# Optimization experiments

Hardware: AMD Instinct MI355X
Metric: run time of the kernel (lower is better)

Reference implementation:

```python
import jax, jax.numpy as jnp
import numpy as np

N = 50000
E = 800000
FEAT = 512
HID = 256
CLS = 40
EPS = 1e-5


def setup_inputs() -> dict:
    key = jax.random.key(0)
    ks = jax.random.split(key, 8)
    x = jax.random.normal(ks[0], (N, FEAT), dtype=jnp.float32)
    edge_index = jax.random.randint(ks[1], (2, E), 0, N, dtype=jnp.int64)
    s = 0.05
    return {
        "x": x,
        "edge_index": edge_index,
        "W1": jax.random.normal(ks[2], (FEAT, HID), dtype=jnp.float32) * s,
        "b1": jnp.zeros((HID,), jnp.float32),
        "W2": jax.random.normal(ks[3], (HID, HID), dtype=jnp.float32) * s,
        "b2": jnp.zeros((HID,), jnp.float32),
        "W3": jax.random.normal(ks[4], (HID, CLS), dtype=jnp.float32) * s,
        "b3": jnp.zeros((CLS,), jnp.float32),
        "gamma": jnp.ones((HID,), jnp.float32),
        "beta": jnp.zeros((HID,), jnp.float32),
        "run_mean": jnp.zeros((HID,), jnp.float32),
        "run_var": jnp.ones((HID,), jnp.float32),
    }


def _edge_norm(edge_index):
    # add self-loops, then symmetric normalization D^-1/2 (A+I) D^-1/2
    loop = jnp.arange(N, dtype=edge_index.dtype)
    src = jnp.concatenate([edge_index[0], loop])
    dst = jnp.concatenate([edge_index[1], loop])
    deg = jax.ops.segment_sum(jnp.ones_like(dst, jnp.float32), dst, num_segments=N)
    inv_sqrt = jnp.where(deg > 0, jax.lax.rsqrt(jnp.maximum(deg, 1.0)), 0.0)
    norm = inv_sqrt[src] * inv_sqrt[dst]  # [E+N]
    return src, dst, norm


def _gcn_conv(x, W, b, src, dst, norm):
    h = x @ W                               # [N, out]
    msg = h[src] * norm[:, None]            # gather + scale, [E+N, out]
    out = jax.ops.segment_sum(msg, dst, num_segments=N)
    return out + b


def _bn_relu(x, gamma, beta, mean, var):
    return jax.nn.relu((x - mean) * jax.lax.rsqrt(var + EPS) * gamma + beta)


def reference(x, edge_index, W1, b1, W2, b2, W3, b3, gamma, beta, run_mean, run_var):
    src, dst, norm = _edge_norm(edge_index)
    h = _gcn_conv(x, W1, b1, src, dst, norm)
    h = _bn_relu(h, gamma, beta, run_mean, run_var)
    h = _gcn_conv(h, W2, b2, src, dst, norm)
    h = _bn_relu(h, gamma, beta, run_mean, run_var)
    h = _gcn_conv(h, W3, b3, src, dst, norm)
    return h
```

## Files before the change

kernel.cpp:

```cpp
#include <hip/hip_runtime.h>
#include <cstdint>
#include <cstddef>

#define FEAT 512
#define HID 256
#define CLS 40
#define EPS 1e-5f

typedef __attribute__((ext_vector_type(8))) short short8;
typedef __attribute__((ext_vector_type(4))) float f32x4v;


__device__ __forceinline__ unsigned short f2bf(float f) {
    union { float f; unsigned u; } v; v.f = f;
    unsigned r = v.u + 0x7FFF + ((v.u >> 16) & 1);
    return (unsigned short)(r >> 16);
}
__device__ __forceinline__ float bf2f(unsigned short h) {
    union { unsigned u; float f; } v; v.u = ((unsigned)h) << 16;
    return v.f;
}

typedef const __attribute__((address_space(1))) unsigned int* gas_ptr;
typedef __attribute__((address_space(3))) unsigned int* las_ptr;
__device__ __forceinline__ void lds_load16(const void* g, void* l) {
    __builtin_amdgcn_global_load_lds((gas_ptr)g, (las_ptr)l, 16, 0, 0);
}

__device__ __forceinline__ void split_f8(float4 a, float4 b, short8& hi, short8& lo) {
    float f[8] = {a.x, a.y, a.z, a.w, b.x, b.y, b.z, b.w};
#pragma unroll
    for (int i = 0; i < 8; ++i) {
        unsigned short h = f2bf(f[i]);
        hi[i] = (short)h;
        lo[i] = (short)f2bf(f[i] - bf2f(h));
    }
}

__device__ __forceinline__ float4 f4add(float4 a, float4 b) {
    return make_float4(a.x + b.x, a.y + b.y, a.z + b.z, a.w + b.w);
}

__device__ __forceinline__ void accum_bf4(float4& a, ushort4 v) {
    a.x += bf2f(v.x); a.y += bf2f(v.y); a.z += bf2f(v.z); a.w += bf2f(v.w);
}


__global__ void zero_kernel(int* counts, int* fillpos, int n) {
    int i = blockIdx.x * 256 + threadIdx.x;
    if (i < n) { counts[i] = 0; fillpos[i] = 0; }
}

__global__ void hist_kernel(const int* __restrict__ dst, int* __restrict__ counts, int E) {
    int e = blockIdx.x * 256 + threadIdx.x;
    if (e < E) atomicAdd(&counts[dst[e]], 1);
}

__global__ void scan_block_kernel(const int* __restrict__ counts, int* __restrict__ row_ptr,
                                  int* __restrict__ blocksums, int n) {
    __shared__ int s[256];
    int tid = threadIdx.x;
    int i = blockIdx.x * 256 + tid;
    int v = (i < n) ? counts[i] : 0;
    s[tid] = v; __syncthreads();
    for (int off = 1; off < 256; off <<= 1) {
        int t = (tid >= off) ? s[tid - off] : 0;
        __syncthreads();
        s[tid] += t;
        __syncthreads();
    }
    if (i < n) row_ptr[i] = s[tid] - v;
    if (tid == 255) blocksums[blockIdx.x] = s[255];
}

__global__ void scan_sums_kernel(const int* __restrict__ blocksums, int* __restrict__ blockoffs, int nb) {
    __shared__ int s[256];
    int tid = threadIdx.x;
    int v = (tid < nb) ? blocksums[tid] : 0;
    s[tid] = v; __syncthreads();
    for (int off = 1; off < 256; off <<= 1) {
        int t = (tid >= off) ? s[tid - off] : 0;
        __syncthreads();
        s[tid] += t;
        __syncthreads();
    }
    blockoffs[tid] = s[tid] - v;
}

__global__ void finalize_rowptr_kernel(int* __restrict__ row_ptr, const int* __restrict__ blockoffs,
                                       const int* __restrict__ counts, float* __restrict__ inv_sqrt,
                                       int n, int E) {
    int i = blockIdx.x * 256 + threadIdx.x;
    if (i < n) {
        row_ptr[i] += blockoffs[i >> 8];
        inv_sqrt[i] = rsqrtf((float)(counts[i] + 1));
    }
    if (i == 0) row_ptr[n] = E;
}

__global__ void fill_kernel(const int* __restrict__ src, const int* __restrict__ dst,
                            const int* __restrict__ row_ptr, int* __restrict__ fillpos,
                            int* __restrict__ src_sorted, int E) {
    int e = blockIdx.x * 256 + threadIdx.x;
    if (e < E) {
        int d = dst[e];
        int pos = row_ptr[d] + atomicAdd(&fillpos[d], 1);
        src_sorted[pos] = src[e];
    }
}


__global__ void cvt_w_kernel(const float* __restrict__ W, unsigned short* __restrict__ hi,
                             unsigned short* __restrict__ lo, int K, int Ncol) {
    int idx = blockIdx.x * 256 + threadIdx.x;
    if (idx >= K * Ncol) return;
    int k = idx / Ncol, n = idx % Ncol;
    float f = W[idx];
    unsigned short h = f2bf(f);
    hi[(size_t)n * K + k] = h;
    lo[(size_t)n * K + k] = f2bf(f - bf2f(h));
}


template<bool A_SPLIT>
__global__ __launch_bounds__(256) void gemm_mfma_kernel(
        const float* __restrict__ Afp,
        const unsigned short* __restrict__ gAhi, const unsigned short* __restrict__ gAlo,
        const unsigned short* __restrict__ Wthi, const unsigned short* __restrict__ Wtlo,
        const float* __restrict__ inv_sqrt, unsigned short* __restrict__ C,
        int M, int K, int Ncol) {
    __shared__ unsigned short AhiL[4096], AloL[4096], BhiL[4096], BloL[4096];
    const int tid  = threadIdx.x;
    const int lane = tid & 63;
    const int w    = tid >> 6;
    const int wr   = w >> 1, wc = w & 1;
    const int lm   = lane & 15;
    const int lk8  = (lane >> 4) * 8;
    const int bm   = blockIdx.x * 128;
    const int bn   = blockIdx.y * 128;

    f32x4v acc[4][4] = {};

    int nc0 = bn + 16 * (2 * w) + lm;
    int nc1 = bn + 16 * (2 * w + 1) + lm;
    const unsigned short* gB_h0 = Wthi + (size_t)nc0 * K + lk8;
    const unsigned short* gB_h1 = Wthi + (size_t)nc1 * K + lk8;
    const unsigned short* gB_l0 = Wtlo + (size_t)nc0 * K + lk8;
    const unsigned short* gB_l1 = Wtlo + (size_t)nc1 * K + lk8;

    int ar0 = bm + 16 * (2 * w) + lm;     if (ar0 >= M) ar0 = M - 1;
    int ar1 = bm + 16 * (2 * w + 1) + lm; if (ar1 >= M) ar1 = M - 1;
    const unsigned short* gA_h0 = gAhi ? gAhi + (size_t)ar0 * K + lk8 : nullptr;
    const unsigned short* gA_h1 = gAhi ? gAhi + (size_t)ar1 * K + lk8 : nullptr;
    const unsigned short* gA_l0 = gAlo ? gAlo + (size_t)ar0 * K + lk8 : nullptr;
    const unsigned short* gA_l1 = gAlo ? gAlo + (size_t)ar1 * K + lk8 : nullptr;

    const int cb = tid >> 5;
    const int cs = tid & 31;
    int crow = bm + 16 * cb + (cs & 15); if (crow >= M) crow = M - 1;
    const int ck = (cs >> 4) * 8;
    const float* Abase = Afp ? Afp + (size_t)crow * K + ck : nullptr;
    unsigned short* ldsA_hi = &AhiL[cb * 512 + 8 * cs];
    unsigned short* ldsA_lo = &AloL[cb * 512 + 8 * cs];

    for (int k0 = 0; k0 < K; k0 += 32) {
        if (A_SPLIT) {
            lds_load16(gA_h0 + k0, &AhiL[(2 * w) * 512]);
            lds_load16(gA_h1 + k0, &AhiL[(2 * w + 1) * 512]);
            lds_load16(gA_l0 + k0, &AloL[(2 * w) * 512]);
            lds_load16(gA_l1 + k0, &AloL[(2 * w + 1) * 512]);
        } else {
            float4 a0 = *(const float4*)(Abase + k0);
            float4 a1 = *(const float4*)(Abase + k0 + 4);
            float4 c0 = *(const float4*)(Abase + k0 + 16);
            float4 c1 = *(const float4*)(Abase + k0 + 20);
            short8 h0, l0, h1, l1;
            split_f8(a0, a1, h0, l0);
            split_f8(c0, c1, h1, l1);
            *(short8*)ldsA_hi         = h0;
            *(short8*)(ldsA_hi + 256) = h1;
            *(short8*)ldsA_lo         = l0;
            *(short8*)(ldsA_lo + 256) = l1;
        }
        lds_load16(gB_h0 + k0, &BhiL[(2 * w) * 512]);
        lds_load16(gB_h1 + k0, &BhiL[(2 * w + 1) * 512]);
        lds_load16(gB_l0 + k0, &BloL[(2 * w) * 512]);
        lds_load16(gB_l1 + k0, &BloL[(2 * w + 1) * 512]);
        __syncthreads();

        short8 ah[4], av[4], bh[4], bv[4];
#pragma unroll
        for (int i = 0; i < 4; ++i) {
            int ao = (wr * 4 + i) * 512 + lane * 8;
            int bo = (wc * 4 + i) * 512 + lane * 8;
            ah[i] = *(const short8*)&AhiL[ao];
            av[i] = *(const short8*)&AloL[ao];
            bh[i] = *(const short8*)&BhiL[bo];
            bv[i] = *(const short8*)&BloL[bo];
        }
#pragma unroll
        for (int i = 0; i < 4; ++i)
#pragma unroll
            for (int j = 0; j < 4; ++j) {
                acc[i][j] = __builtin_amdgcn_mfma_f32_16x16x32_bf16(ah[i], bh[j], acc[i][j], 0, 0, 0);
                acc[i][j] = __builtin_amdgcn_mfma_f32_16x16x32_bf16(av[i], bh[j], acc[i][j], 0, 0, 0);
                acc[i][j] = __builtin_amdgcn_mfma_f32_16x16x32_bf16(ah[i], bv[j], acc[i][j], 0, 0, 0);
            }
        __syncthreads();
    }

    const int orow_base = bm + wr * 64;
    const int ocol_base = bn + wc * 64 + lm;
    const int rq = (lane >> 4) * 4;
#pragma unroll
    for (int i = 0; i < 4; ++i) {
#pragma unroll
        for (int r = 0; r < 4; ++r) {
            int row = orow_base + i * 16 + rq + r;
            if (row >= M) continue;
            float s = inv_sqrt[row];
            size_t rb = (size_t)row * Ncol;
#pragma unroll
            for (int j = 0; j < 4; ++j)
                C[rb + ocol_base + j * 16] = f2bf(acc[i][j][r] * s);
        }
    }
}


__global__ __launch_bounds__(256) void gemm_scaled_hl_kernel(
        const unsigned short* __restrict__ Ahi, const unsigned short* __restrict__ Alo,
        const float* __restrict__ W,
        const float* __restrict__ inv_sqrt, float* __restrict__ C,
        int M, int K, int Ncol) {
    __shared__ float As[16][64];
    __shared__ float Ws[16][64];
    int tid = threadIdx.x;
    int tm = tid >> 4;
    int tn = tid & 15;
    int bm = blockIdx.x * 64;
    int bn = blockIdx.y * 64;

    float acc[4][4] = {};

    int lr = tid >> 2;
    int lc = (tid & 3) << 2;
    int wr = tid >> 4;
    int wc = (tid & 15) << 2;
    int arow = bm + lr;
    bool aok = arow < M;
    bool wok = (bn + wc) < Ncol;
    const unsigned short* AhiRow = Ahi + (size_t)arow * K + lc;
    const unsigned short* AloRow = Alo + (size_t)arow * K + lc;

    for (int k0 = 0; k0 < K; k0 += 16) {
        float4 av = make_float4(0.f, 0.f, 0.f, 0.f);
        if (aok) {
            ushort4 hv = *(const ushort4*)(AhiRow + k0);
            ushort4 lv = *(const ushort4*)(AloRow + k0);
            av.x = bf2f(hv.x) + bf2f(lv.x);
            av.y = bf2f(hv.y) + bf2f(lv.y);
            av.z = bf2f(hv.z) + bf2f(lv.z);
            av.w = bf2f(hv.w) + bf2f(lv.w);
        }
        As[lc + 0][lr] = av.x; As[lc + 1][lr] = av.y;
        As[lc + 2][lr] = av.z; As[lc + 3][lr] = av.w;

        float4 wv = make_float4(0.f, 0.f, 0.f, 0.f);
        if (wok) wv = *(const float4*)(W + (size_t)(k0 + wr) * Ncol + bn + wc);
        *(float4*)&Ws[wr][wc] = wv;
        __syncthreads();

#pragma unroll
        for (int k = 0; k < 16; ++k) {
            const float4 a4 = *(const float4*)&As[k][tm << 2];
            const float4 b4 = *(const float4*)&Ws[k][tn << 2];
            float a[4] = {a4.x, a4.y, a4.z, a4.w};
            float b[4] = {b4.x, b4.y, b4.z, b4.w};
#pragma unroll
            for (int i = 0; i < 4; ++i)
#pragma unroll
                for (int j = 0; j < 4; ++j)
                    acc[i][j] = fmaf(a[i], b[j], acc[i][j]);
        }
        __syncthreads();
    }

#pragma unroll
    for (int i = 0; i < 4; ++i) {
        int row = bm + (tm << 2) + i;
        if (row >= M) continue;
        float s = inv_sqrt[row];
        int col = bn + (tn << 2);
        if (col < Ncol) {
            float4 o = make_float4(acc[i][0] * s, acc[i][1] * s, acc[i][2] * s, acc[i][3] * s);
            *(float4*)&C[(size_t)row * Ncol + col] = o;
        }
    }
}


__global__ __launch_bounds__(256) void agg_bn_hl_kernel(
        const unsigned short* __restrict__ g, const int* __restrict__ row_ptr,
        const int* __restrict__ srcs, const float* __restrict__ inv_sqrt,
        const float* __restrict__ bias, const float* __restrict__ gamma,
        const float* __restrict__ beta, const float* __restrict__ mean,
        const float* __restrict__ var,
        unsigned short* __restrict__ out_hi, unsigned short* __restrict__ out_lo, int n) {
    int node = (blockIdx.x << 2) + (threadIdx.x >> 6);
    int lane = threadIdx.x & 63;
    if (node >= n) return;
    const ushort4* gp = (const ushort4*)g;
    float4 acc0 = make_float4(0.f, 0.f, 0.f, 0.f);
    float4 acc1 = make_float4(0.f, 0.f, 0.f, 0.f);
    accum_bf4(acc0, gp[(size_t)node * 64 + lane]);
    int beg = row_ptr[node];
    int cnt = row_ptr[node + 1] - beg;

    for (int base = 0; base < cnt; base += 64) {
        int m = cnt - base; if (m > 64) m = 64;
        int idx = (lane < m) ? srcs[beg + base + lane] : 0;
        int j = 0;
        for (; j + 8 <= m; j += 8) {
            int s0 = __shfl(idx, j + 0), s1 = __shfl(idx, j + 1);
            int s2 = __shfl(idx, j + 2), s3 = __shfl(idx, j + 3);
            int s4 = __shfl(idx, j + 4), s5 = __shfl(idx, j + 5);
            int s6 = __shfl(idx, j + 6), s7 = __shfl(idx, j + 7);
            ushort4 v0 = gp[(size_t)s0 * 64 + lane];
            ushort4 v1 = gp[(size_t)s1 * 64 + lane];
            ushort4 v2 = gp[(size_t)s2 * 64 + lane];
            ushort4 v3 = gp[(size_t)s3 * 64 + lane];
            ushort4 v4 = gp[(size_t)s4 * 64 + lane];
            ushort4 v5 = gp[(size_t)s5 * 64 + lane];
            ushort4 v6 = gp[(size_t)s6 * 64 + lane];
            ushort4 v7 = gp[(size_t)s7 * 64 + lane];
            accum_bf4(acc0, v0); accum_bf4(acc0, v1);
            accum_bf4(acc0, v2); accum_bf4(acc0, v3);
            accum_bf4(acc1, v4); accum_bf4(acc1, v5);
            accum_bf4(acc1, v6); accum_bf4(acc1, v7);
        }
        for (; j < m; ++j) {
            int s = __shfl(idx, j);
            accum_bf4(acc0, gp[(size_t)s * 64 + lane]);
        }
    }
    float4 acc = f4add(acc0, acc1);

    float inv = inv_sqrt[node];
    float4 b4  = ((const float4*)bias)[lane];
    float4 ga4 = ((const float4*)gamma)[lane];
    float4 be4 = ((const float4*)beta)[lane];
    float4 m4  = ((const float4*)mean)[lane];
    float4 v4  = ((const float4*)var)[lane];
    float4 o;
    o.x = fmaxf((acc.x * inv + b4.x - m4.x) * (ga4.x * rsqrtf(v4.x + EPS)) + be4.x, 0.f);
    o.y = fmaxf((acc.y * inv + b4.y - m4.y) * (ga4.y * rsqrtf(v4.y + EPS)) + be4.y, 0.f);
    o.z = fmaxf((acc.z * inv + b4.z - m4.z) * (ga4.z * rsqrtf(v4.z + EPS)) + be4.z, 0.f);
    o.w = fmaxf((acc.w * inv + b4.w - m4.w) * (ga4.w * rsqrtf(v4.w + EPS)) + be4.w, 0.f);
    ushort4 oh, ol;
    oh.x = f2bf(o.x); ol.x = f2bf(o.x - bf2f(oh.x));
    oh.y = f2bf(o.y); ol.y = f2bf(o.y - bf2f(oh.y));
    oh.z = f2bf(o.z); ol.z = f2bf(o.z - bf2f(oh.z));
    oh.w = f2bf(o.w); ol.w = f2bf(o.w - bf2f(oh.w));
    ((ushort4*)out_hi)[(size_t)node * 64 + lane] = oh;
    ((ushort4*)out_lo)[(size_t)node * 64 + lane] = ol;
}


__global__ __launch_bounds__(256) void agg_final_kernel(
        const float* __restrict__ g, const int* __restrict__ row_ptr,
        const int* __restrict__ srcs, const float* __restrict__ inv_sqrt,
        const float* __restrict__ bias, float* __restrict__ out, int n) {
    int node = (blockIdx.x << 2) + (threadIdx.x >> 6);
    int lane = threadIdx.x & 63;
    if (node >= n) return;
    int flane = (lane < CLS) ? lane : 0;
    float acc0 = g[(size_t)node * CLS + flane];
    float acc1 = 0.f;
    int beg = row_ptr[node];
    int cnt = row_ptr[node + 1] - beg;

    for (int base = 0; base < cnt; base += 64) {
        int m = cnt - base; if (m > 64) m = 64;
        int idx = (lane < m) ? srcs[beg + base + lane] : 0;
        int j = 0;
        for (; j + 8 <= m; j += 8) {
            int s0 = __shfl(idx, j + 0), s1 = __shfl(idx, j + 1);
            int s2 = __shfl(idx, j + 2), s3 = __shfl(idx, j + 3);
            int s4 = __shfl(idx, j + 4), s5 = __shfl(idx, j + 5);
            int s6 = __shfl(idx, j + 6), s7 = __shfl(idx, j + 7);
            float v0 = g[(size_t)s0 * CLS + flane];
            float v1 = g[(size_t)s1 * CLS + flane];
            float v2 = g[(size_t)s2 * CLS + flane];
            float v3 = g[(size_t)s3 * CLS + flane];
            float v4 = g[(size_t)s4 * CLS + flane];
            float v5 = g[(size_t)s5 * CLS + flane];
            float v6 = g[(size_t)s6 * CLS + flane];
            float v7 = g[(size_t)s7 * CLS + flane];
            acc0 += (v0 + v1) + (v2 + v3);
            acc1 += (v4 + v5) + (v6 + v7);
        }
        for (; j < m; ++j) {
            int s = __shfl(idx, j);
            acc0 += g[(size_t)s * CLS + flane];
        }
    }
    if (lane < CLS)
        out[(size_t)node * CLS + lane] = (acc0 + acc1) * inv_sqrt[node] + bias[lane];
}


extern "C" void kernel_launch(void* const* d_in, const int* in_sizes, int n_in,
                              void* d_out, int out_size, void* d_ws, size_t ws_size,
                              hipStream_t stream) {
    const float* x     = (const float*)d_in[0];
    const int*   edges = (const int*)d_in[1];
    const float* W1    = (const float*)d_in[2];
    const float* b1    = (const float*)d_in[3];
    const float* W2    = (const float*)d_in[4];
    const float* b2    = (const float*)d_in[5];
    const float* W3    = (const float*)d_in[6];
    const float* b3    = (const float*)d_in[7];
    const float* gamma = (const float*)d_in[8];
    const float* beta  = (const float*)d_in[9];
    const float* mean  = (const float*)d_in[10];
    const float* var   = (const float*)d_in[11];

    const int N = in_sizes[0] / FEAT;
    const int E = in_sizes[1] / 2;
    const int* src = edges;
    const int* dst = edges + E;

    char* ws = (char*)d_ws;
    auto alloc = [&](size_t bytes) -> char* {
        char* p = ws;
        ws += (bytes + 255) & ~(size_t)255;
        return p;
    };
    int*   counts     = (int*)  alloc((size_t)N * 4);
    int*   fillpos    = (int*)  alloc((size_t)N * 4);
    int*   row_ptr    = (int*)  alloc((size_t)(N + 1) * 4);
    int*   blocksums  = (int*)  alloc(256 * 4);
    int*   blockoffs  = (int*)  alloc(256 * 4);
    float* inv_sqrt   = (float*)alloc((size_t)N * 4);
    int*   src_sorted = (int*)  alloc((size_t)E * 4);
    unsigned short* w1hi = (unsigned short*)alloc((size_t)FEAT * HID * 2);
    unsigned short* w1lo = (unsigned short*)alloc((size_t)FEAT * HID * 2);
    unsigned short* w2hi = (unsigned short*)alloc((size_t)HID * HID * 2);
    unsigned short* w2lo = (unsigned short*)alloc((size_t)HID * HID * 2);
    unsigned short* g    = (unsigned short*)alloc((size_t)N * HID * 2);
    unsigned short* h_hi = (unsigned short*)alloc((size_t)N * HID * 2);
    unsigned short* h_lo = (unsigned short*)alloc((size_t)N * HID * 2);

    int nb = (N + 255) / 256;
    int eb = (E + 255) / 256;

    zero_kernel<<<nb, 256, 0, stream>>>(counts, fillpos, N);
    hist_kernel<<<eb, 256, 0, stream>>>(dst, counts, E);
    scan_block_kernel<<<nb, 256, 0, stream>>>(counts, row_ptr, blocksums, N);
    scan_sums_kernel<<<1, 256, 0, stream>>>(blocksums, blockoffs, nb);
    finalize_rowptr_kernel<<<nb, 256, 0, stream>>>(row_ptr, blockoffs, counts, inv_sqrt, N, E);
    fill_kernel<<<eb, 256, 0, stream>>>(src, dst, row_ptr, fillpos, src_sorted, E);

    cvt_w_kernel<<<(FEAT * HID + 255) / 256, 256, 0, stream>>>(W1, w1hi, w1lo, FEAT, HID);
    cvt_w_kernel<<<(HID * HID + 255) / 256, 256, 0, stream>>>(W2, w2hi, w2lo, HID, HID);

    dim3 mfma_grid((N + 127) / 128, HID / 128);
    dim3 gemm3_grid((N + 63) / 64, 1);
    dim3 agg_grid((N + 3) / 4);

    gemm_mfma_kernel<false><<<mfma_grid, 256, 0, stream>>>(
        x, nullptr, nullptr, w1hi, w1lo, inv_sqrt, g, N, FEAT, HID);
    agg_bn_hl_kernel<<<agg_grid, 256, 0, stream>>>(g, row_ptr, src_sorted, inv_sqrt,
                                                   b1, gamma, beta, mean, var, h_hi, h_lo, N);
    gemm_mfma_kernel<true><<<mfma_grid, 256, 0, stream>>>(
        nullptr, h_hi, h_lo, w2hi, w2lo, inv_sqrt, g, N, HID, HID);
    agg_bn_hl_kernel<<<agg_grid, 256, 0, stream>>>(g, row_ptr, src_sorted, inv_sqrt,
                                                   b2, gamma, beta, mean, var, h_hi, h_lo, N);
    float* g3 = (float*)g;
    gemm_scaled_hl_kernel<<<gemm3_grid, 256, 0, stream>>>(h_hi, h_lo, W3, inv_sqrt, g3, N, HID, CLS);
    agg_final_kernel<<<agg_grid, 256, 0, stream>>>(g3, row_ptr, src_sorted, inv_sqrt,
                                                   b3, (float*)d_out, N);
}
```

Before: 550.0 us.

## Pre-convert x to bf16 in a separate pass and drop A low-part MFMA in layer 1

Adds a standalone kernel that converts x to bf16 (high part only) into a reused buffer. The first GEMM then loads A through global_load_lds instead of converting fp32 in the inner loop, and drops the A-low correction MFMA and its LDS buffer. This cuts the per-tile conversion ALU work, a third of the layer-1 MFMAs, and LDS footprint. In exchange it adds an extra read and write pass over x and loses the low-order bits of x, so layer-1 precision drops.

```diff
diff --git a/kernel.cpp b/kernel.cpp
--- a/kernel.cpp
+++ b/kernel.cpp
@@ -25,16 +25,6 @@
 typedef __attribute__((address_space(3))) unsigned int* las_ptr;
 __device__ __forceinline__ void lds_load16(const void* g, void* l) {
     __builtin_amdgcn_global_load_lds((gas_ptr)g, (las_ptr)l, 16, 0, 0);
-}
-
-__device__ __forceinline__ void split_f8(float4 a, float4 b, short8& hi, short8& lo) {
-    float f[8] = {a.x, a.y, a.z, a.w, b.x, b.y, b.z, b.w};
-#pragma unroll
-    for (int i = 0; i < 8; ++i) {
-        unsigned short h = f2bf(f[i]);
-        hi[i] = (short)h;
-        lo[i] = (short)f2bf(f[i] - bf2f(h));
-    }
 }
 
 __device__ __forceinline__ float4 f4add(float4 a, float4 b) {
@@ -122,14 +112,29 @@
 }
 
 
+__global__ __launch_bounds__(256) void cvt_x_kernel(const float* __restrict__ x,
+                                                    unsigned short* __restrict__ out, int total8) {
+    int i = blockIdx.x * 256 + threadIdx.x;
+    if (i >= total8) return;
+    const float4* xp = (const float4*)x;
+    float4 a = xp[2 * i], b = xp[2 * i + 1];
+    float f[8] = {a.x, a.y, a.z, a.w, b.x, b.y, b.z, b.w};
+    short8 h;
+#pragma unroll
+    for (int j = 0; j < 8; ++j) h[j] = (short)f2bf(f[j]);
+    ((short8*)out)[i] = h;
+}
+
+
 template<bool A_SPLIT>
 __global__ __launch_bounds__(256) void gemm_mfma_kernel(
-        const float* __restrict__ Afp,
         const unsigned short* __restrict__ gAhi, const unsigned short* __restrict__ gAlo,
         const unsigned short* __restrict__ Wthi, const unsigned short* __restrict__ Wtlo,
         const float* __restrict__ inv_sqrt, unsigned short* __restrict__ C,
         int M, int K, int Ncol) {
-    __shared__ unsigned short AhiL[4096], AloL[4096], BhiL[4096], BloL[4096];
+    __shared__ unsigned short AhiL[4096];
+    __shared__ unsigned short AloL[A_SPLIT ? 4096 : 4];
+    __shared__ unsigned short BhiL[4096], BloL[4096];
     const int tid  = threadIdx.x;
     const int lane = tid & 63;
     const int w    = tid >> 6;
@@ -150,37 +155,17 @@
 
     int ar0 = bm + 16 * (2 * w) + lm;     if (ar0 >= M) ar0 = M - 1;
     int ar1 = bm + 16 * (2 * w + 1) + lm; if (ar1 >= M) ar1 = M - 1;
-    const unsigned short* gA_h0 = gAhi ? gAhi + (size_t)ar0 * K + lk8 : nullptr;
-    const unsigned short* gA_h1 = gAhi ? gAhi + (size_t)ar1 * K + lk8 : nullptr;
-    const unsigned short* gA_l0 = gAlo ? gAlo + (size_t)ar0 * K + lk8 : nullptr;
-    const unsigned short* gA_l1 = gAlo ? gAlo + (size_t)ar1 * K + lk8 : nullptr;
-
-    const int cb = tid >> 5;
-    const int cs = tid & 31;
-    int crow = bm + 16 * cb + (cs & 15); if (crow >= M) crow = M - 1;
-    const int ck = (cs >> 4) * 8;
-    const float* Abase = Afp ? Afp + (size_t)crow * K + ck : nullptr;
-    unsigned short* ldsA_hi = &AhiL[cb * 512 + 8 * cs];
-    unsigned short* ldsA_lo = &AloL[cb * 512 + 8 * cs];
+    const unsigned short* gA_h0 = gAhi + (size_t)ar0 * K + lk8;
+    const unsigned short* gA_h1 = gAhi + (size_t)ar1 * K + lk8;
+    const unsigned short* gA_l0 = A_SPLIT ? gAlo + (size_t)ar0 * K + lk8 : nullptr;
+    const unsigned short* gA_l1 = A_SPLIT ? gAlo + (size_t)ar1 * K + lk8 : nullptr;
 
     for (int k0 = 0; k0 < K; k0 += 32) {
+        lds_load16(gA_h0 + k0, &AhiL[(2 * w) * 512]);
+        lds_load16(gA_h1 + k0, &AhiL[(2 * w + 1) * 512]);
         if (A_SPLIT) {
-            lds_load16(gA_h0 + k0, &AhiL[(2 * w) * 512]);
-            lds_load16(gA_h1 + k0, &AhiL[(2 * w + 1) * 512]);
             lds_load16(gA_l0 + k0, &AloL[(2 * w) * 512]);
             lds_load16(gA_l1 + k0, &AloL[(2 * w + 1) * 512]);
-        } else {
-            float4 a0 = *(const float4*)(Abase + k0);
-            float4 a1 = *(const float4*)(Abase + k0 + 4);
-            float4 c0 = *(const float4*)(Abase + k0 + 16);
-            float4 c1 = *(const float4*)(Abase + k0 + 20);
-            short8 h0, l0, h1, l1;
-            split_f8(a0, a1, h0, l0);
-            split_f8(c0, c1, h1, l1);
-            *(short8*)ldsA_hi         = h0;
-            *(short8*)(ldsA_hi + 256) = h1;
-            *(short8*)ldsA_lo         = l0;
-            *(short8*)(ldsA_lo + 256) = l1;
         }
         lds_load16(gB_h0 + k0, &BhiL[(2 * w) * 512]);
         lds_load16(gB_h1 + k0, &BhiL[(2 * w + 1) * 512]);
@@ -194,7 +179,7 @@
             int ao = (wr * 4 + i) * 512 + lane * 8;
             int bo = (wc * 4 + i) * 512 + lane * 8;
             ah[i] = *(const short8*)&AhiL[ao];
-            av[i] = *(const short8*)&AloL[ao];
+            if (A_SPLIT) av[i] = *(const short8*)&AloL[ao];
             bh[i] = *(const short8*)&BhiL[bo];
             bv[i] = *(const short8*)&BloL[bo];
         }
@@ -203,7 +188,8 @@
 #pragma unroll
             for (int j = 0; j < 4; ++j) {
                 acc[i][j] = __builtin_amdgcn_mfma_f32_16x16x32_bf16(ah[i], bh[j], acc[i][j], 0, 0, 0);
-                acc[i][j] = __builtin_amdgcn_mfma_f32_16x16x32_bf16(av[i], bh[j], acc[i][j], 0, 0, 0);
+                if (A_SPLIT)
+                    acc[i][j] = __builtin_amdgcn_mfma_f32_16x16x32_bf16(av[i], bh[j], acc[i][j], 0, 0, 0);
                 acc[i][j] = __builtin_amdgcn_mfma_f32_16x16x32_bf16(ah[i], bv[j], acc[i][j], 0, 0, 0);
             }
         __syncthreads();
@@ -451,6 +437,7 @@
     unsigned short* g    = (unsigned short*)alloc((size_t)N * HID * 2);
     unsigned short* h_hi = (unsigned short*)alloc((size_t)N * HID * 2);
     unsigned short* h_lo = (unsigned short*)alloc((size_t)N * HID * 2);
+    unsigned short* xbf  = h_hi;
 
     int nb = (N + 255) / 256;
     int eb = (E + 255) / 256;
@@ -464,17 +451,19 @@
 
     cvt_w_kernel<<<(FEAT * HID + 255) / 256, 256, 0, stream>>>(W1, w1hi, w1lo, FEAT, HID);
     cvt_w_kernel<<<(HID * HID + 255) / 256, 256, 0, stream>>>(W2, w2hi, w2lo, HID, HID);
+    int total8 = N * FEAT / 8;
+    cvt_x_kernel<<<(total8 + 255) / 256, 256, 0, stream>>>(x, xbf, total8);
 
     dim3 mfma_grid((N + 127) / 128, HID / 128);
     dim3 gemm3_grid((N + 63) / 64, 1);
     dim3 agg_grid((N + 3) / 4);
 
     gemm_mfma_kernel<false><<<mfma_grid, 256, 0, stream>>>(
-        x, nullptr, nullptr, w1hi, w1lo, inv_sqrt, g, N, FEAT, HID);
+        xbf, nullptr, w1hi, w1lo, inv_sqrt, g, N, FEAT, HID);
     agg_bn_hl_kernel<<<agg_grid, 256, 0, stream>>>(g, row_ptr, src_sorted, inv_sqrt,
                                                    b1, gamma, beta, mean, var, h_hi, h_lo, N);
     gemm_mfma_kernel<true><<<mfma_grid, 256, 0, stream>>>(
-        nullptr, h_hi, h_lo, w2hi, w2lo, inv_sqrt, g, N, HID, HID);
+        h_hi, h_lo, w2hi, w2lo, inv_sqrt, g, N, HID, HID);
     agg_bn_hl_kernel<<<agg_grid, 256, 0, stream>>>(g, row_ptr, src_sorted, inv_sqrt,
                                                    b2, gamma, beta, mean, var, h_hi, h_lo, N);
     float* g3 = (float*)g;
```

After: 564.5 us. 2.6% more time.
